# Kernel optimization log

Measured on AMD Instinct MI355X. Metric: run time of the kernel, lower is better.

The kernel has to match this reference:

```python
import jax, jax.numpy as jnp
import numpy as np

B, L, Q, K, H = 64, 1024, 1024, 1024, 1024

def setup_inputs() -> dict:
    key = jax.random.key(0)
    k1, k2, k3, k4, k5, k6 = jax.random.split(key, 6)
    query = jax.random.normal(k1, (B, Q), dtype=jnp.float32)
    keys = jax.random.normal(k2, (B, L, K), dtype=jnp.float32)
    mask = jax.random.randint(k3, (B, L), 0, 2).astype(bool)
    # nn.Linear weights: W1 [H, Q], W2 [H, K], v [1, H], all bias-free
    W1 = jax.random.normal(k4, (H, Q), dtype=jnp.float32) / np.sqrt(Q)
    W2 = jax.random.normal(k5, (H, K), dtype=jnp.float32) / np.sqrt(K)
    v = jax.random.normal(k6, (1, H), dtype=jnp.float32) / np.sqrt(H)
    return {"query": query, "keys": keys, "mask": mask, "W1": W1, "W2": W2, "v": v}

def reference(query, keys, mask, W1, W2, v):
    # q: [B, H], broadcast over seq dim instead of expand
    q = query @ W1.T                                  # [B, H]
    k = jnp.einsum('blk,hk->blh', keys, W2)           # [B, L, H]
    scores = jnp.tanh(q[:, None, :] + k) @ v[0]       # [B, L]
    scores = jnp.where(mask, -jnp.inf, scores)
    weights = jax.nn.softmax(scores, axis=-1)
    weights = jnp.nan_to_num(weights, nan=0.0)
    context = jnp.einsum('bl,blk->bk', weights, keys) # [B, K]
    return (context, weights)
```

## Files before the change

### kernel.cpp

```cpp
#include <hip/hip_runtime.h>
#include <math.h>


typedef __attribute__((ext_vector_type(8))) short short8;
typedef __attribute__((ext_vector_type(4))) float floatx4;

__device__ __forceinline__ short f2bf(float x) {
    unsigned u = __float_as_uint(x);
    u += 0x7fffu + ((u >> 16) & 1u);
    return (short)(u >> 16);
}
__device__ __forceinline__ short8 pack8(float4 lo, float4 hi) {
    short8 r;
    r[0]=f2bf(lo.x); r[1]=f2bf(lo.y); r[2]=f2bf(lo.z); r[3]=f2bf(lo.w);
    r[4]=f2bf(hi.x); r[5]=f2bf(hi.y); r[6]=f2bf(hi.z); r[7]=f2bf(hi.w);
    return r;
}

#define LDA 40

__global__ __launch_bounds__(256) void k0_zero(float* __restrict__ out) {
    const int i = (blockIdx.x * 256 + threadIdx.x) * 4;
    const float4 z = {0.f, 0.f, 0.f, 0.f};
    *(float4*)(out + i) = z;
}

__global__ __launch_bounds__(256) void k1_qproj(
    const float* __restrict__ query, const float* __restrict__ W1,
    float* __restrict__ out)
{
    __shared__ float As[32][64];
    __shared__ float Bs[32][64];
    const int t  = threadIdx.x;
    const int tx = t & 15, ty = t >> 4;
    const int h0 = blockIdx.x * 64;
    const int kbase = blockIdx.y * 256;
    const int sr = t >> 2;
    const int sk = (t & 3) * 8;
    float c[4][4] = {{0.f}};
    for (int k0 = kbase; k0 < kbase + 256; k0 += 32) {
        const float4 a0 = *(const float4*)(query + sr * 1024 + k0 + sk);
        const float4 a1 = *(const float4*)(query + sr * 1024 + k0 + sk + 4);
        const float4 b0 = *(const float4*)(W1 + (h0 + sr) * 1024 + k0 + sk);
        const float4 b1 = *(const float4*)(W1 + (h0 + sr) * 1024 + k0 + sk + 4);
        __syncthreads();
        As[sk+0][sr]=a0.x; As[sk+1][sr]=a0.y; As[sk+2][sr]=a0.z; As[sk+3][sr]=a0.w;
        As[sk+4][sr]=a1.x; As[sk+5][sr]=a1.y; As[sk+6][sr]=a1.z; As[sk+7][sr]=a1.w;
        Bs[sk+0][sr]=b0.x; Bs[sk+1][sr]=b0.y; Bs[sk+2][sr]=b0.z; Bs[sk+3][sr]=b0.w;
        Bs[sk+4][sr]=b1.x; Bs[sk+5][sr]=b1.y; Bs[sk+6][sr]=b1.z; Bs[sk+7][sr]=b1.w;
        __syncthreads();
        #pragma unroll
        for (int k = 0; k < 32; ++k) {
            const float4 av = *(const float4*)&As[k][ty*4];
            const float4 bv = *(const float4*)&Bs[k][tx*4];
            const float aa[4] = {av.x, av.y, av.z, av.w};
            const float bb[4] = {bv.x, bv.y, bv.z, bv.w};
            #pragma unroll
            for (int i = 0; i < 4; ++i)
                #pragma unroll
                for (int j = 0; j < 4; ++j)
                    c[i][j] = fmaf(aa[i], bb[j], c[i][j]);
        }
    }
    #pragma unroll
    for (int i = 0; i < 4; ++i)
        #pragma unroll
        for (int j = 0; j < 4; ++j)
            atomicAdd(&out[(ty*4 + i) * 1024 + h0 + tx*4 + j], c[i][j]);
}

__global__ __launch_bounds__(256) void k_pack(const float* __restrict__ src,
                                              short* __restrict__ dst, int nunits)
{
    const int stride = gridDim.x * 256;
    for (int o = blockIdx.x * 256 + threadIdx.x; o < nunits; o += stride) {
        const int m = o & 15;
        const int c = (o >> 4) & 127;
        const int panel = o >> 11;
        const size_t f = ((size_t)panel * 16 + m) * 1024 + c * 8;
        const float4 a = *(const float4*)(src + f);
        const float4 b = *(const float4*)(src + f + 4);
        ((short8*)dst)[o] = pack8(a, b);
    }
}

__global__ __launch_bounds__(256) void k2_scores_direct(
    const short* __restrict__ keysp, const short* __restrict__ W2p,
    const float* __restrict__ v, float* __restrict__ out)
{
    __shared__ float red[128][33];
    const int t  = threadIdx.x;
    const int hb = blockIdx.x;
    const int l0 = blockIdx.y * 128;
    const int b  = blockIdx.z;
    const int h0 = hb * 128;
    const float* q = out;
    float* score = out + 65536;

    const int lane = t & 63, wid = t >> 6;
    const int quad = lane >> 4, m16 = lane & 15;
    const int wm = (wid >> 1) * 64;
    const int wn = (wid & 1) * 64;

    const short8* pA = (const short8*)keysp
        + ((size_t)(b * 64 + (l0 >> 4) + (wm >> 4))) * 2048 + quad * 16 + m16;
    const short8* pB = (const short8*)W2p
        + ((size_t)((h0 >> 4) + (wn >> 4))) * 2048 + quad * 16 + m16;

    floatx4 acc[4][4] = {};
    short8 a0[4], b0[4], a1[4], b1[4];

    #pragma unroll
    for (int i = 0; i < 4; ++i) { a0[i] = pA[i * 2048]; b0[i] = pB[i * 2048]; }

    for (int kk = 0; kk < 928; kk += 64) {
        #pragma unroll
        for (int i = 0; i < 4; ++i) {
            a1[i] = pA[i * 2048 + (kk + 32) * 2];
            b1[i] = pB[i * 2048 + (kk + 32) * 2];
        }
        #pragma unroll
        for (int i = 0; i < 4; ++i)
            #pragma unroll
            for (int j = 0; j < 4; ++j)
                acc[i][j] = __builtin_amdgcn_mfma_f32_16x16x32_bf16(a0[i], b0[j], acc[i][j], 0, 0, 0);
        #pragma unroll
        for (int i = 0; i < 4; ++i) {
            a0[i] = pA[i * 2048 + (kk + 64) * 2];
            b0[i] = pB[i * 2048 + (kk + 64) * 2];
        }
        #pragma unroll
        for (int i = 0; i < 4; ++i)
            #pragma unroll
            for (int j = 0; j < 4; ++j)
                acc[i][j] = __builtin_amdgcn_mfma_f32_16x16x32_bf16(a1[i], b1[j], acc[i][j], 0, 0, 0);
    }
    #pragma unroll
    for (int i = 0; i < 4; ++i) {
        a1[i] = pA[i * 2048 + 992 * 2];
        b1[i] = pB[i * 2048 + 992 * 2];
    }
    #pragma unroll
    for (int i = 0; i < 4; ++i)
        #pragma unroll
        for (int j = 0; j < 4; ++j)
            acc[i][j] = __builtin_amdgcn_mfma_f32_16x16x32_bf16(a0[i], b0[j], acc[i][j], 0, 0, 0);
    #pragma unroll
    for (int i = 0; i < 4; ++i)
        #pragma unroll
        for (int j = 0; j < 4; ++j)
            acc[i][j] = __builtin_amdgcn_mfma_f32_16x16x32_bf16(a1[i], b1[j], acc[i][j], 0, 0, 0);

    float qv[4], vv[4];
    #pragma unroll
    for (int j = 0; j < 4; ++j) {
        const int h = h0 + wn + j * 16 + m16;
        qv[j] = q[b * 1024 + h];
        vv[j] = v[h];
    }
    #pragma unroll
    for (int i = 0; i < 4; ++i) {
        #pragma unroll
        for (int r = 0; r < 4; ++r) {
            float s = 0.f;
            #pragma unroll
            for (int j = 0; j < 4; ++j)
                s += tanhf(qv[j] + acc[i][j][r]) * vv[j];
            red[wm + i * 16 + quad * 4 + r][(wid & 1) * 16 + m16] = s;
        }
    }
    __syncthreads();
    if (t < 128) {
        const float* rr = red[t];
        float s = 0.f;
        #pragma unroll
        for (int c = 0; c < 32; ++c) s += rr[c];
        atomicAdd(&score[b * 1024 + l0 + t], s);
    }
}

__global__ __launch_bounds__(256) void k2_scores(
    const float* __restrict__ keys, const float* __restrict__ W2,
    const float* __restrict__ v, float* __restrict__ out)
{
    __shared__ union {
        struct { short A[128][LDA]; short B[128][LDA]; } st;
        float red[128][33];
    } sm;
    const int t  = threadIdx.x;
    const int hb = blockIdx.x;
    const int l0 = blockIdx.y * 128;
    const int b  = blockIdx.z;
    const int h0 = hb * 128;
    const float* q = out;
    float* score = out + 65536;

    const int srow = t >> 1;
    const int skh  = (t & 1) * 16;
    const float* Arow = keys + ((size_t)(b * 1024 + l0 + srow)) * 1024 + skh;
    const float* Brow = W2   + ((size_t)(h0 + srow)) * 1024 + skh;

    const int lane = t & 63, wid = t >> 6;
    const int quad = lane >> 4, m16 = lane & 15;
    const int wm = (wid >> 1) * 64;
    const int wn = (wid & 1) * 64;

    floatx4 acc[4][4] = {};

    for (int kk = 0; kk < 1024; kk += 32) {
        const float4 a0 = *(const float4*)(Arow + kk);
        const float4 a1 = *(const float4*)(Arow + kk + 4);
        const float4 a2 = *(const float4*)(Arow + kk + 8);
        const float4 a3 = *(const float4*)(Arow + kk + 12);
        const float4 w0 = *(const float4*)(Brow + kk);
        const float4 w1 = *(const float4*)(Brow + kk + 4);
        const float4 w2 = *(const float4*)(Brow + kk + 8);
        const float4 w3 = *(const float4*)(Brow + kk + 12);
        __syncthreads();
        *(short8*)&sm.st.A[srow][skh]     = pack8(a0, a1);
        *(short8*)&sm.st.A[srow][skh + 8] = pack8(a2, a3);
        *(short8*)&sm.st.B[srow][skh]     = pack8(w0, w1);
        *(short8*)&sm.st.B[srow][skh + 8] = pack8(w2, w3);
        __syncthreads();
        short8 af[4], bf[4];
        #pragma unroll
        for (int i = 0; i < 4; ++i)
            af[i] = *(const short8*)&sm.st.A[wm + i*16 + m16][quad * 8];
        #pragma unroll
        for (int j = 0; j < 4; ++j)
            bf[j] = *(const short8*)&sm.st.B[wn + j*16 + m16][quad * 8];
        #pragma unroll
        for (int i = 0; i < 4; ++i)
            #pragma unroll
            for (int j = 0; j < 4; ++j)
                acc[i][j] = __builtin_amdgcn_mfma_f32_16x16x32_bf16(af[i], bf[j], acc[i][j], 0, 0, 0);
    }

    float qv[4], vv[4];
    #pragma unroll
    for (int j = 0; j < 4; ++j) {
        const int h = h0 + wn + j * 16 + m16;
        qv[j] = q[b * 1024 + h];
        vv[j] = v[h];
    }
    __syncthreads();
    #pragma unroll
    for (int i = 0; i < 4; ++i) {
        #pragma unroll
        for (int r = 0; r < 4; ++r) {
            float s = 0.f;
            #pragma unroll
            for (int j = 0; j < 4; ++j)
                s += tanhf(qv[j] + acc[i][j][r]) * vv[j];
            sm.red[wm + i * 16 + quad * 4 + r][(wid & 1) * 16 + m16] = s;
        }
    }
    __syncthreads();
    if (t < 128) {
        const float* rr = sm.red[t];
        float s = 0.f;
        #pragma unroll
        for (int c = 0; c < 32; ++c) s += rr[c];
        atomicAdd(&score[b * 1024 + l0 + t], s);
    }
}

__global__ __launch_bounds__(256) void k3_softmax(
    const unsigned char* __restrict__ mask_u8, float* __restrict__ out)
{
    __shared__ float sc[1024];
    __shared__ float red[256];
    __shared__ int nz_sh;
    const int b = blockIdx.x;
    const int t = threadIdx.x;

    if (t == 0) nz_sh = 0;
    __syncthreads();
    {
        int nz = 0;
        #pragma unroll
        for (int j = 1; j < 4; ++j)
            if (mask_u8[t * 4 + j] != 0) nz = 1;
        if (nz) atomicAdd(&nz_sh, 1);
    }
    __syncthreads();
    const int use_i32 = (nz_sh == 0);
    const int* mask_i32 = (const int*)mask_u8;

    float* score = out + 65536;
    float lmax = -INFINITY;
    #pragma unroll
    for (int i = 0; i < 4; ++i) {
        const int l = t + i * 256;
        float s = score[b * 1024 + l];
        const int ml = b * 1024 + l;
        const bool masked = use_i32 ? (mask_i32[ml] != 0) : (mask_u8[ml] != 0);
        if (masked) s = -INFINITY;
        sc[l] = s;
        lmax = fmaxf(lmax, s);
    }
    red[t] = lmax;
    __syncthreads();
    for (int off = 128; off > 0; off >>= 1) {
        if (t < off) red[t] = fmaxf(red[t], red[t + off]);
        __syncthreads();
    }
    const float m = red[0];
    __syncthreads();
    float e[4];
    float lsum = 0.f;
    #pragma unroll
    for (int i = 0; i < 4; ++i) {
        const float s = sc[t + i * 256];
        const float ev = (s > -INFINITY && m > -INFINITY) ? expf(s - m) : 0.f;
        e[i] = ev;
        lsum += ev;
    }
    red[t] = lsum;
    __syncthreads();
    for (int off = 128; off > 0; off >>= 1) {
        if (t < off) red[t] += red[t + off];
        __syncthreads();
    }
    const float S = red[0];
    const float inv = (S > 0.f) ? (1.f / S) : 0.f;
    #pragma unroll
    for (int i = 0; i < 4; ++i)
        score[b * 1024 + t + i * 256] = e[i] * inv;
    const float4 z = {0.f, 0.f, 0.f, 0.f};
    ((float4*)(out + b * 1024))[t] = z;
}

__global__ __launch_bounds__(256) void k4_context(
    const float* __restrict__ keys, float* __restrict__ out)
{
    __shared__ float w[128];
    const int t  = threadIdx.x;
    const int b  = blockIdx.y;
    const int l0 = blockIdx.x * 128;
    if (t < 128) w[t] = out[65536 + b * 1024 + l0 + t];
    __syncthreads();
    const float4* kp = (const float4*)(keys + ((size_t)b * 1024 + (size_t)l0) * 1024) + t;
    float4 acc = {0.f, 0.f, 0.f, 0.f};
    #pragma unroll 4
    for (int l = 0; l < 128; ++l) {
        const float4 kv = kp[(size_t)l * 256];
        const float wv = w[l];
        acc.x = fmaf(wv, kv.x, acc.x);
        acc.y = fmaf(wv, kv.y, acc.y);
        acc.z = fmaf(wv, kv.z, acc.z);
        acc.w = fmaf(wv, kv.w, acc.w);
    }
    float* o = out + b * 1024 + t * 4;
    atomicAdd(o + 0, acc.x);
    atomicAdd(o + 1, acc.y);
    atomicAdd(o + 2, acc.z);
    atomicAdd(o + 3, acc.w);
}

extern "C" void kernel_launch(void* const* d_in, const int* in_sizes, int n_in,
                              void* d_out, int out_size, void* d_ws, size_t ws_size,
                              hipStream_t stream) {
    const float*         query = (const float*)d_in[0];
    const float*         keys  = (const float*)d_in[1];
    const unsigned char* mask  = (const unsigned char*)d_in[2];
    const float*         W1    = (const float*)d_in[3];
    const float*         W2    = (const float*)d_in[4];
    const float*         v     = (const float*)d_in[5];
    float* out = (float*)d_out;

    const size_t KEYS_BF = (size_t)64 * 1024 * 1024 * 2;
    const size_t W2_BF   = (size_t)1024 * 1024 * 2;
    const bool use_ws = (d_ws != nullptr) && (ws_size >= KEYS_BF + W2_BF);

    k0_zero   <<<dim3(128),       256, 0, stream>>>(out);
    k1_qproj  <<<dim3(16, 4),     256, 0, stream>>>(query, W1, out);
    if (use_ws) {
        short* keysp = (short*)d_ws;
        short* W2p   = keysp + KEYS_BF / 2;
        k_pack<<<dim3(2048), 256, 0, stream>>>(keys, keysp, 8388608);
        k_pack<<<dim3(512),  256, 0, stream>>>(W2,   W2p,   131072);
        k2_scores_direct<<<dim3(8, 8, 64), 256, 0, stream>>>(keysp, W2p, v, out);
    } else {
        k2_scores       <<<dim3(8, 8, 64), 256, 0, stream>>>(keys, W2, v, out);
    }
    k3_softmax<<<dim3(64),        256, 0, stream>>>(mask, out);
    k4_context<<<dim3(8, 64),     256, 0, stream>>>(keys, out);
}
```

Baseline: 667.1 us.

## Use row-major bf16 conversion, reorder scores grid, and use fast tanh

Replaces the panel-swizzled bf16 packing with a plain row-major fp32-to-bf16 conversion, and rewrites the MFMA scores kernel to load fragments with per-row pointers. The grid is reordered so the h-block index is slowest, meaning consecutive blocks cover different l and b tiles while sharing the same W2 slice. tanhf is replaced with an exp plus reciprocal approximation to cut transcendental cost in the epilogue. The row-major layout gives strided 16-byte fragment loads instead of contiguous panel reads, which may hurt coalescing, and the fast tanh may lose accuracy for large arguments.

```diff
diff --git a/kernel.cpp b/kernel.cpp
--- a/kernel.cpp
+++ b/kernel.cpp
@@ -15,6 +15,10 @@
     r[0]=f2bf(lo.x); r[1]=f2bf(lo.y); r[2]=f2bf(lo.z); r[3]=f2bf(lo.w);
     r[4]=f2bf(hi.x); r[5]=f2bf(hi.y); r[6]=f2bf(hi.z); r[7]=f2bf(hi.w);
     return r;
+}
+__device__ __forceinline__ float fast_tanh(float x) {
+    const float e = __expf(2.f * x);
+    return 1.f - 2.f * __builtin_amdgcn_rcpf(e + 1.f);
 }
 
 #define LDA 40
@@ -69,30 +73,26 @@
             atomicAdd(&out[(ty*4 + i) * 1024 + h0 + tx*4 + j], c[i][j]);
 }
 
-__global__ __launch_bounds__(256) void k_pack(const float* __restrict__ src,
-                                              short* __restrict__ dst, int nunits)
+__global__ __launch_bounds__(256) void k_cvt(const float* __restrict__ src,
+                                             short* __restrict__ dst, int n8)
 {
     const int stride = gridDim.x * 256;
-    for (int o = blockIdx.x * 256 + threadIdx.x; o < nunits; o += stride) {
-        const int m = o & 15;
-        const int c = (o >> 4) & 127;
-        const int panel = o >> 11;
-        const size_t f = ((size_t)panel * 16 + m) * 1024 + c * 8;
-        const float4 a = *(const float4*)(src + f);
-        const float4 b = *(const float4*)(src + f + 4);
-        ((short8*)dst)[o] = pack8(a, b);
+    for (int i = blockIdx.x * 256 + threadIdx.x; i < n8; i += stride) {
+        const float4 a = ((const float4*)src)[(size_t)i * 2];
+        const float4 b = ((const float4*)src)[(size_t)i * 2 + 1];
+        ((short8*)dst)[i] = pack8(a, b);
     }
 }
 
 __global__ __launch_bounds__(256) void k2_scores_direct(
-    const short* __restrict__ keysp, const short* __restrict__ W2p,
+    const short* __restrict__ keysb, const short* __restrict__ W2b,
     const float* __restrict__ v, float* __restrict__ out)
 {
     __shared__ float red[128][33];
     const int t  = threadIdx.x;
-    const int hb = blockIdx.x;
-    const int l0 = blockIdx.y * 128;
-    const int b  = blockIdx.z;
+    const int l0 = blockIdx.x * 128;
+    const int b  = blockIdx.y;
+    const int hb = blockIdx.z;
     const int h0 = hb * 128;
     const float* q = out;
     float* score = out + 65536;
@@ -102,33 +102,31 @@
     const int wm = (wid >> 1) * 64;
     const int wn = (wid & 1) * 64;
 
-    const short8* pA = (const short8*)keysp
-        + ((size_t)(b * 64 + (l0 >> 4) + (wm >> 4))) * 2048 + quad * 16 + m16;
-    const short8* pB = (const short8*)W2p
-        + ((size_t)((h0 >> 4) + (wn >> 4))) * 2048 + quad * 16 + m16;
+    const short8* pa[4];
+    const short8* pb[4];
+    #pragma unroll
+    for (int i = 0; i < 4; ++i) {
+        pa[i] = (const short8*)keysb + ((size_t)(b * 1024 + l0 + wm + i * 16 + m16)) * 128 + quad;
+        pb[i] = (const short8*)W2b   + ((size_t)(h0 + wn + i * 16 + m16)) * 128 + quad;
+    }
 
     floatx4 acc[4][4] = {};
     short8 a0[4], b0[4], a1[4], b1[4];
 
     #pragma unroll
-    for (int i = 0; i < 4; ++i) { a0[i] = pA[i * 2048]; b0[i] = pB[i * 2048]; }
-
-    for (int kk = 0; kk < 928; kk += 64) {
-        #pragma unroll
-        for (int i = 0; i < 4; ++i) {
-            a1[i] = pA[i * 2048 + (kk + 32) * 2];
-            b1[i] = pB[i * 2048 + (kk + 32) * 2];
-        }
+    for (int i = 0; i < 4; ++i) { a0[i] = pa[i][0]; b0[i] = pb[i][0]; }
+
+    #pragma unroll
+    for (int kc = 0; kc < 120; kc += 8) {
+        #pragma unroll
+        for (int i = 0; i < 4; ++i) { a1[i] = pa[i][kc + 4]; b1[i] = pb[i][kc + 4]; }
         #pragma unroll
         for (int i = 0; i < 4; ++i)
             #pragma unroll
             for (int j = 0; j < 4; ++j)
                 acc[i][j] = __builtin_amdgcn_mfma_f32_16x16x32_bf16(a0[i], b0[j], acc[i][j], 0, 0, 0);
         #pragma unroll
-        for (int i = 0; i < 4; ++i) {
-            a0[i] = pA[i * 2048 + (kk + 64) * 2];
-            b0[i] = pB[i * 2048 + (kk + 64) * 2];
-        }
+        for (int i = 0; i < 4; ++i) { a0[i] = pa[i][kc + 8]; b0[i] = pb[i][kc + 8]; }
         #pragma unroll
         for (int i = 0; i < 4; ++i)
             #pragma unroll
@@ -136,10 +134,7 @@
                 acc[i][j] = __builtin_amdgcn_mfma_f32_16x16x32_bf16(a1[i], b1[j], acc[i][j], 0, 0, 0);
     }
     #pragma unroll
-    for (int i = 0; i < 4; ++i) {
-        a1[i] = pA[i * 2048 + 992 * 2];
-        b1[i] = pB[i * 2048 + 992 * 2];
-    }
+    for (int i = 0; i < 4; ++i) { a1[i] = pa[i][124]; b1[i] = pb[i][124]; }
     #pragma unroll
     for (int i = 0; i < 4; ++i)
         #pragma unroll
@@ -165,7 +160,7 @@
             float s = 0.f;
             #pragma unroll
             for (int j = 0; j < 4; ++j)
-                s += tanhf(qv[j] + acc[i][j][r]) * vv[j];
+                s += fast_tanh(qv[j] + acc[i][j][r]) * vv[j];
             red[wm + i * 16 + quad * 4 + r][(wid & 1) * 16 + m16] = s;
         }
     }
@@ -376,11 +371,11 @@
     k0_zero   <<<dim3(128),       256, 0, stream>>>(out);
     k1_qproj  <<<dim3(16, 4),     256, 0, stream>>>(query, W1, out);
     if (use_ws) {
-        short* keysp = (short*)d_ws;
-        short* W2p   = keysp + KEYS_BF / 2;
-        k_pack<<<dim3(2048), 256, 0, stream>>>(keys, keysp, 8388608);
-        k_pack<<<dim3(512),  256, 0, stream>>>(W2,   W2p,   131072);
-        k2_scores_direct<<<dim3(8, 8, 64), 256, 0, stream>>>(keysp, W2p, v, out);
+        short* keysb = (short*)d_ws;
+        short* W2b   = keysb + KEYS_BF / 2;
+        k_cvt <<<dim3(2048), 256, 0, stream>>>(keys, keysb, 8388608);
+        k_cvt <<<dim3(512),  256, 0, stream>>>(W2,   W2b,   131072);
+        k2_scores_direct<<<dim3(8, 64, 8), 256, 0, stream>>>(keysb, W2b, v, out);
     } else {
         k2_scores       <<<dim3(8, 8, 64), 256, 0, stream>>>(keys, W2, v, out);
     }
```

New measurement: 931.6 us. 39.7% more time.

## Loop all hidden blocks per scores workgroup and use fast tanh

Applied to the files above, without the earlier changes.

The packed-workspace scores kernel now loops over all eight hidden-dimension blocks inside one workgroup instead of launching a separate workgroup per block. Partial scores accumulate in registers and are written directly, so the atomics and the zeroing of the score region go away. tanhf is replaced with an exp plus reciprocal approximation in both scores kernels. The grid shrinks from 4096 to 512 workgroups, which may reduce latency hiding on a large GPU, and the fast tanh may lose accuracy or overflow for large inputs.

```diff
diff --git a/kernel.cpp b/kernel.cpp
--- a/kernel.cpp
+++ b/kernel.cpp
@@ -15,6 +15,10 @@
     r[0]=f2bf(lo.x); r[1]=f2bf(lo.y); r[2]=f2bf(lo.z); r[3]=f2bf(lo.w);
     r[4]=f2bf(hi.x); r[5]=f2bf(hi.y); r[6]=f2bf(hi.z); r[7]=f2bf(hi.w);
     return r;
+}
+__device__ __forceinline__ float fast_tanh(float x) {
+    const float e = __expf(2.f * x);
+    return 1.f - 2.f * __builtin_amdgcn_rcpf(e + 1.f);
 }
 
 #define LDA 40
@@ -84,16 +88,14 @@
     }
 }
 
-__global__ __launch_bounds__(256) void k2_scores_direct(
+__global__ __launch_bounds__(256) void k2_scores_full(
     const short* __restrict__ keysp, const short* __restrict__ W2p,
     const float* __restrict__ v, float* __restrict__ out)
 {
     __shared__ float red[128][33];
     const int t  = threadIdx.x;
-    const int hb = blockIdx.x;
-    const int l0 = blockIdx.y * 128;
-    const int b  = blockIdx.z;
-    const int h0 = hb * 128;
+    const int l0 = blockIdx.x * 128;
+    const int b  = blockIdx.y;
     const float* q = out;
     float* score = out + 65536;
 
@@ -104,20 +106,44 @@
 
     const short8* pA = (const short8*)keysp
         + ((size_t)(b * 64 + (l0 >> 4) + (wm >> 4))) * 2048 + quad * 16 + m16;
-    const short8* pB = (const short8*)W2p
-        + ((size_t)((h0 >> 4) + (wn >> 4))) * 2048 + quad * 16 + m16;
-
-    floatx4 acc[4][4] = {};
-    short8 a0[4], b0[4], a1[4], b1[4];
-
-    #pragma unroll
-    for (int i = 0; i < 4; ++i) { a0[i] = pA[i * 2048]; b0[i] = pB[i * 2048]; }
-
-    for (int kk = 0; kk < 928; kk += 64) {
+
+    float s_loc[4][4] = {{0.f}};
+
+    for (int hb = 0; hb < 8; ++hb) {
+        const short8* pB = (const short8*)W2p
+            + ((size_t)(hb * 8 + (wn >> 4))) * 2048 + quad * 16 + m16;
+
+        floatx4 acc[4][4] = {};
+        short8 a0[4], b0[4], a1[4], b1[4];
+        #pragma unroll
+        for (int i = 0; i < 4; ++i) { a0[i] = pA[i * 2048]; b0[i] = pB[i * 2048]; }
+
+        for (int kk = 0; kk < 928; kk += 64) {
+            #pragma unroll
+            for (int i = 0; i < 4; ++i) {
+                a1[i] = pA[i * 2048 + (kk + 32) * 2];
+                b1[i] = pB[i * 2048 + (kk + 32) * 2];
+            }
+            #pragma unroll
+            for (int i = 0; i < 4; ++i)
+                #pragma unroll
+                for (int j = 0; j < 4; ++j)
+                    acc[i][j] = __builtin_amdgcn_mfma_f32_16x16x32_bf16(a0[i], b0[j], acc[i][j], 0, 0, 0);
+            #pragma unroll
+            for (int i = 0; i < 4; ++i) {
+                a0[i] = pA[i * 2048 + (kk + 64) * 2];
+                b0[i] = pB[i * 2048 + (kk + 64) * 2];
+            }
+            #pragma unroll
+            for (int i = 0; i < 4; ++i)
+                #pragma unroll
+                for (int j = 0; j < 4; ++j)
+                    acc[i][j] = __builtin_amdgcn_mfma_f32_16x16x32_bf16(a1[i], b1[j], acc[i][j], 0, 0, 0);
+        }
         #pragma unroll
         for (int i = 0; i < 4; ++i) {
-            a1[i] = pA[i * 2048 + (kk + 32) * 2];
-            b1[i] = pB[i * 2048 + (kk + 32) * 2];
+            a1[i] = pA[i * 2048 + 992 * 2];
+            b1[i] = pB[i * 2048 + 992 * 2];
         }
         #pragma unroll
         for (int i = 0; i < 4; ++i)
@@ -125,57 +151,42 @@
             for (int j = 0; j < 4; ++j)
                 acc[i][j] = __builtin_amdgcn_mfma_f32_16x16x32_bf16(a0[i], b0[j], acc[i][j], 0, 0, 0);
         #pragma unroll
-        for (int i = 0; i < 4; ++i) {
-            a0[i] = pA[i * 2048 + (kk + 64) * 2];
-            b0[i] = pB[i * 2048 + (kk + 64) * 2];
-        }
-        #pragma unroll
         for (int i = 0; i < 4; ++i)
             #pragma unroll
             for (int j = 0; j < 4; ++j)
                 acc[i][j] = __builtin_amdgcn_mfma_f32_16x16x32_bf16(a1[i], b1[j], acc[i][j], 0, 0, 0);
-    }
-    #pragma unroll
-    for (int i = 0; i < 4; ++i) {
-        a1[i] = pA[i * 2048 + 992 * 2];
-        b1[i] = pB[i * 2048 + 992 * 2];
-    }
+
+        float qv[4], vv[4];
+        #pragma unroll
+        for (int j = 0; j < 4; ++j) {
+            const int h = hb * 128 + wn + j * 16 + m16;
+            qv[j] = q[b * 1024 + h];
+            vv[j] = v[h];
+        }
+        #pragma unroll
+        for (int i = 0; i < 4; ++i)
+            #pragma unroll
+            for (int r = 0; r < 4; ++r) {
+                float s = 0.f;
+                #pragma unroll
+                for (int j = 0; j < 4; ++j)
+                    s += fast_tanh(qv[j] + acc[i][j][r]) * vv[j];
+                s_loc[i][r] += s;
+            }
+    }
+
     #pragma unroll
     for (int i = 0; i < 4; ++i)
         #pragma unroll
-        for (int j = 0; j < 4; ++j)
-            acc[i][j] = __builtin_amdgcn_mfma_f32_16x16x32_bf16(a0[i], b0[j], acc[i][j], 0, 0, 0);
-    #pragma unroll
-    for (int i = 0; i < 4; ++i)
-        #pragma unroll
-        for (int j = 0; j < 4; ++j)
-            acc[i][j] = __builtin_amdgcn_mfma_f32_16x16x32_bf16(a1[i], b1[j], acc[i][j], 0, 0, 0);
-
-    float qv[4], vv[4];
-    #pragma unroll
-    for (int j = 0; j < 4; ++j) {
-        const int h = h0 + wn + j * 16 + m16;
-        qv[j] = q[b * 1024 + h];
-        vv[j] = v[h];
-    }
-    #pragma unroll
-    for (int i = 0; i < 4; ++i) {
-        #pragma unroll
-        for (int r = 0; r < 4; ++r) {
-            float s = 0.f;
-            #pragma unroll
-            for (int j = 0; j < 4; ++j)
-                s += tanhf(qv[j] + acc[i][j][r]) * vv[j];
-            red[wm + i * 16 + quad * 4 + r][(wid & 1) * 16 + m16] = s;
-        }
-    }
+        for (int r = 0; r < 4; ++r)
+            red[wm + i * 16 + quad * 4 + r][(wid & 1) * 16 + m16] = s_loc[i][r];
     __syncthreads();
     if (t < 128) {
         const float* rr = red[t];
         float s = 0.f;
         #pragma unroll
         for (int c = 0; c < 32; ++c) s += rr[c];
-        atomicAdd(&score[b * 1024 + l0 + t], s);
+        score[b * 1024 + l0 + t] = s;
     }
 }
 
@@ -251,7 +262,7 @@
             float s = 0.f;
             #pragma unroll
             for (int j = 0; j < 4; ++j)
-                s += tanhf(qv[j] + acc[i][j][r]) * vv[j];
+                s += fast_tanh(qv[j] + acc[i][j][r]) * vv[j];
             sm.red[wm + i * 16 + quad * 4 + r][(wid & 1) * 16 + m16] = s;
         }
     }
@@ -263,6 +274,12 @@
         for (int c = 0; c < 32; ++c) s += rr[c];
         atomicAdd(&score[b * 1024 + l0 + t], s);
     }
+}
+
+__global__ __launch_bounds__(256) void k0_zero_score(float* __restrict__ out) {
+    const int i = (blockIdx.x * 256 + threadIdx.x) * 4;
+    const float4 z = {0.f, 0.f, 0.f, 0.f};
+    *(float4*)(out + 65536 + i) = z;
 }
 
 __global__ __launch_bounds__(256) void k3_softmax(
@@ -373,16 +390,17 @@
     const size_t W2_BF   = (size_t)1024 * 1024 * 2;
     const bool use_ws = (d_ws != nullptr) && (ws_size >= KEYS_BF + W2_BF);
 
-    k0_zero   <<<dim3(128),       256, 0, stream>>>(out);
+    k0_zero   <<<dim3(64),        256, 0, stream>>>(out);
     k1_qproj  <<<dim3(16, 4),     256, 0, stream>>>(query, W1, out);
     if (use_ws) {
         short* keysp = (short*)d_ws;
         short* W2p   = keysp + KEYS_BF / 2;
         k_pack<<<dim3(2048), 256, 0, stream>>>(keys, keysp, 8388608);
         k_pack<<<dim3(512),  256, 0, stream>>>(W2,   W2p,   131072);
-        k2_scores_direct<<<dim3(8, 8, 64), 256, 0, stream>>>(keysp, W2p, v, out);
+        k2_scores_full<<<dim3(8, 64), 256, 0, stream>>>(keysp, W2p, v, out);
     } else {
-        k2_scores       <<<dim3(8, 8, 64), 256, 0, stream>>>(keys, W2, v, out);
+        k0_zero_score<<<dim3(64), 256, 0, stream>>>(out);
+        k2_scores    <<<dim3(8, 8, 64), 256, 0, stream>>>(keys, W2, v, out);
     }
     k3_softmax<<<dim3(64),        256, 0, stream>>>(mask, out);
     k4_context<<<dim3(8, 64),     256, 0, stream>>>(keys, out);
```

Result: no change. 668.9 us (+0.3%).
